# Performance work log

Measured on AMD Instinct MI355X. Metric: run time of the kernel, lower is better.

Reference implementation:

```python
import jax, jax.numpy as jnp
import numpy as np

HIDDEN = 512
HEADS = 8
HEAD_DIM = HIDDEN // HEADS


def setup_inputs() -> dict:
    key = jax.random.key(0)
    ks = jax.random.split(key, 12)
    B, N, C = 4, 2048, HIDDEN
    s = 1.0 / np.sqrt(C)
    inp = {
        "query_content": jax.random.normal(ks[0], (B, N, C), dtype=jnp.float32),
        "query_pos": jax.random.uniform(ks[1], (B, N, 4), dtype=jnp.float32),
        "Wq": jax.random.uniform(ks[2], (C, C), jnp.float32, -s, s),
        "bq": jax.random.uniform(ks[3], (C,), jnp.float32, -s, s),
        "Wk": jax.random.uniform(ks[4], (C, C), jnp.float32, -s, s),
        "bk": jax.random.uniform(ks[5], (C,), jnp.float32, -s, s),
        "Wv": jax.random.uniform(ks[6], (C, C), jnp.float32, -s, s),
        "bv": jax.random.uniform(ks[7], (C,), jnp.float32, -s, s),
        "Wo": jax.random.uniform(ks[8], (C, C), jnp.float32, -s, s),
        "bo": jax.random.uniform(ks[9], (C,), jnp.float32, -s, s),
        "gamma": jnp.ones((C,), jnp.float32),
        "beta": jnp.zeros((C,), jnp.float32),
    }
    return inp


def _iof_bias(query_pos):
    # query_pos: [B, N, 4] -> bias [B, N, N] = -0.1 * sqrt(dx^2 + dy^2 + eps)
    x = query_pos[..., 0]
    y = query_pos[..., 1]
    dx = jnp.abs(x[:, :, None] - x[:, None, :])
    dy = jnp.abs(y[:, :, None] - y[:, None, :])
    dist = jnp.sqrt(dx * dx + dy * dy + 1e-8)
    return -0.1 * dist


def reference(query_content, query_pos, Wq, bq, Wk, bk, Wv, bv, Wo, bo, gamma, beta):
    B, N, C = query_content.shape
    H, D = HEADS, HEAD_DIM
    # torch Linear: x @ W.T + b
    Q = (query_content @ Wq.T + bq).reshape(B, N, H, D).transpose(0, 2, 1, 3)
    K = (query_content @ Wk.T + bk).reshape(B, N, H, D).transpose(0, 2, 1, 3)
    V = (query_content @ Wv.T + bv).reshape(B, N, H, D).transpose(0, 2, 1, 3)
    scores = jnp.einsum("bhnd,bhmd->bhnm", Q, K) / jnp.sqrt(jnp.float32(D))
    scores = scores + _iof_bias(query_pos)[:, None, :, :]
    attn = jax.nn.softmax(scores, axis=-1)
    out = jnp.einsum("bhnm,bhmd->bhnd", attn, V)
    out = out.transpose(0, 2, 1, 3).reshape(B, N, C)
    out = out @ Wo.T + bo
    h = out + query_content
    mu = jnp.mean(h, axis=-1, keepdims=True)
    var = jnp.var(h, axis=-1, keepdims=True)
    return (h - mu) / jnp.sqrt(var + 1e-5) * gamma + beta
```

## Files before the change

### kernel.cpp

```cpp
#include <hip/hip_runtime.h>
#include <hip/hip_bf16.h>

#define C_DIM 512
#define H_NUM 8
#define D_DIM 64
#define B_NUM 4
#define N_SEQ 2048
#define M_TOT (B_NUM*N_SEQ)

typedef unsigned short u16;
typedef unsigned int   u32;
typedef __attribute__((ext_vector_type(8))) short short8;
typedef __attribute__((ext_vector_type(4))) float f32x4;

#define MFMA16 __builtin_amdgcn_mfma_f32_16x16x32_bf16

__device__ __forceinline__ u16 f2b(float f) {
    union { float f; u32 u; } v; v.f = f;
    u32 r = v.u + 0x7FFFu + ((v.u >> 16) & 1u);
    return (u16)(r >> 16);
}
__device__ __forceinline__ float fexp2(float x) {
    float r;
    asm("v_exp_f32 %0, %1" : "=v"(r) : "v"(x));
    return r;
}
__device__ __forceinline__ float b2f_lo(u32 u) {
    union { u32 u; float f; } v; v.u = u << 16; return v.f;
}
__device__ __forceinline__ float b2f_hi(u32 u) {
    union { u32 u; float f; } v; v.u = u & 0xFFFF0000u; return v.f;
}
__device__ __forceinline__ void gload16(const u16* g, u16* l) {
    __builtin_amdgcn_global_load_lds(
        (const __attribute__((address_space(1))) void*)g,
        (__attribute__((address_space(3))) void*)l, 16, 0, 0);
}
__device__ __forceinline__ void cast8(const float* s, u16* d) {
    const float4* p = (const float4*)s;
    float4 a = p[0], b = p[1];
    short8 v;
    v[0] = (short)f2b(a.x); v[1] = (short)f2b(a.y);
    v[2] = (short)f2b(a.z); v[3] = (short)f2b(a.w);
    v[4] = (short)f2b(b.x); v[5] = (short)f2b(b.y);
    v[6] = (short)f2b(b.z); v[7] = (short)f2b(b.w);
    *(short8*)d = v;
}

__global__ __launch_bounds__(256) void k_prep(const float* __restrict__ qc,
                                              const float* __restrict__ Wq,
                                              const float* __restrict__ Wk,
                                              const float* __restrict__ Wv,
                                              const float* __restrict__ Wo,
                                              const float* __restrict__ bq,
                                              const float* __restrict__ bk,
                                              const float* __restrict__ bv,
                                              const float* __restrict__ bo,
                                              const float* __restrict__ qpos,
                                              u16* __restrict__ xb,
                                              u16* __restrict__ wb,
                                              float* __restrict__ bqkv,
                                              u16* __restrict__ bias)
{
    const int bid = blockIdx.x, t = threadIdx.x;
    if (bid < 2048) {
        int i = bid * 256 + t;
        cast8(qc + (size_t)i * 8, xb + (size_t)i * 8);
    } else if (bid < 2560) {
        int r = bid - 2048;
        int y = r >> 7;
        const float* s = (y == 0) ? Wq : (y == 1) ? Wk : (y == 2) ? Wv : Wo;
        int i = (r & 127) * 256 + t;
        cast8(s + (size_t)i * 8, wb + (size_t)y * 262144 + (size_t)i * 8);
    } else if (bid < 2568) {
        int idx = (bid - 2560) * 256 + t;
        float v = idx < 512 ? bq[idx] : idx < 1024 ? bk[idx - 512]
                : idx < 1536 ? bv[idx - 1024] : bo[idx - 1536];
        bqkv[idx] = v;
    } else {
        int r = bid - 2568;
        int i = r & 2047, b = r >> 11;
        const float4 qi = *(const float4*)(qpos + (size_t)(b * 2048 + i) * 4);
        const float4* pj = (const float4*)(qpos + ((size_t)b * 2048 + t * 8) * 4);
        const float NC = -0.1f * 1.4426950408889634f;
        short8 v;
        #pragma unroll
        for (int jj = 0; jj < 8; ++jj) {
            float4 pk = pj[jj];
            float dx = qi.x - pk.x, dy = qi.y - pk.y;
            float d2 = fmaf(dx, dx, fmaf(dy, dy, 1e-8f));
            v[jj] = (short)f2b(sqrtf(d2) * NC);
        }
        *(short8*)(bias + (size_t)(b * 2048 + i) * 2048 + t * 8) = v;
    }
}

__global__ __launch_bounds__(256) void k_gemm(const u16* __restrict__ A,
                                              const u16* __restrict__ Bw,
                                              const float* __restrict__ bias,
                                              u16* __restrict__ oq,
                                              u16* __restrict__ ok,
                                              u16* __restrict__ ov,
                                              float* __restrict__ outf,
                                              int fixed_mode)
{
    __shared__ alignas(16) u16 la[4][128][8];
    __shared__ alignas(16) u16 lb[4][128][8];
    const int t = threadIdx.x;
    const int nwg = gridDim.x * gridDim.y;
    const int wgid = blockIdx.y * gridDim.x + blockIdx.x;
    const int swz = (wgid & 7) * (nwg >> 3) + (wgid >> 3);
    const int ntn = gridDim.y;
    const int m0 = (swz / ntn) * 128, n0 = (swz % ntn) * 128;
    const int w = t >> 6, l = t & 63, lr = l & 15, kg = l >> 4;
    const int wm = w >> 1, wn = w & 1;

    f32x4 acc[4][4] = {};

    const int srow = t & 127;
    const u16* As0 = A + (size_t)(m0 + srow) * C_DIM + (t >> 7) * 8;
    const u16* Bs0 = Bw + (size_t)(n0 + srow) * C_DIM + (t >> 7) * 8;
    u16* ldA = (u16*)la + w * 512;
    u16* ldB = (u16*)lb + w * 512;

    for (int k0 = 0; k0 < C_DIM; k0 += 32) {
        gload16(As0 + k0,      ldA);
        gload16(As0 + k0 + 16, ldA + 2048);
        gload16(Bs0 + k0,      ldB);
        gload16(Bs0 + k0 + 16, ldB + 2048);
        __syncthreads();

        short8 af[4], bf[4];
        #pragma unroll
        for (int fm = 0; fm < 4; ++fm)
            af[fm] = *(const short8*)la[kg][wm * 64 + fm * 16 + lr];
        #pragma unroll
        for (int fn = 0; fn < 4; ++fn)
            bf[fn] = *(const short8*)lb[kg][wn * 64 + fn * 16 + lr];
        #pragma unroll
        for (int fm = 0; fm < 4; ++fm)
        #pragma unroll
        for (int fn = 0; fn < 4; ++fn)
            acc[fm][fn] = MFMA16(af[fm], bf[fn], acc[fm][fn], 0, 0, 0);
        __syncthreads();
    }

    const int mode = (fixed_mode == 3) ? 3 : (n0 >> 9);

    if (mode == 3) {
        #pragma unroll
        for (int fm = 0; fm < 4; ++fm)
        #pragma unroll
        for (int fn = 0; fn < 4; ++fn) {
            int c = n0 + wn * 64 + fn * 16 + lr;
            float bv_ = bias[c];
            #pragma unroll
            for (int i = 0; i < 4; ++i) {
                int m = m0 + wm * 64 + fm * 16 + kg * 4 + i;
                outf[(size_t)m * C_DIM + c] = acc[fm][fn][i] + bv_;
            }
        }
    } else if (mode == 2) {
        #pragma unroll
        for (int fm = 0; fm < 4; ++fm)
        #pragma unroll
        for (int fn = 0; fn < 4; ++fn) {
            int c = n0 + wn * 64 + fn * 16 + lr;
            int cc = c & 511, h = cc >> 6, d = cc & 63;
            float bv_ = bias[c];
            int m = m0 + wm * 64 + fm * 16 + kg * 4;
            int bb = m >> 11, n = m & 2047;
            uint2 pk;
            pk.x = ((u32)f2b(acc[fm][fn][1] + bv_) << 16) | f2b(acc[fm][fn][0] + bv_);
            pk.y = ((u32)f2b(acc[fm][fn][3] + bv_) << 16) | f2b(acc[fm][fn][2] + bv_);
            *(uint2*)(ov + ((size_t)(bb * H_NUM + h) * D_DIM + d) * N_SEQ + n) = pk;
        }
    } else {
        u16* outb = (mode == 0) ? oq : ok;
        #pragma unroll
        for (int fm = 0; fm < 4; ++fm)
        #pragma unroll
        for (int fn = 0; fn < 4; ++fn) {
            int c = n0 + wn * 64 + fn * 16 + lr;
            int cc = c & 511, h = cc >> 6, d = cc & 63;
            float bv_ = bias[c];
            #pragma unroll
            for (int i = 0; i < 4; ++i) {
                int m = m0 + wm * 64 + fm * 16 + kg * 4 + i;
                int bb = m >> 11, n = m & 2047;
                outb[((size_t)(bb * H_NUM + h) * N_SEQ + n) * D_DIM + d] = f2b(bv_ + acc[fm][fn][i]);
            }
        }
    }
}

__global__ __launch_bounds__(512, 4) void k_flash(const u16* __restrict__ Q,
                                                  const u16* __restrict__ K,
                                                  const u16* __restrict__ Vt,
                                                  const u16* __restrict__ bias,
                                                  u16* __restrict__ attn_out)
{
    __shared__ alignas(16) u16 kbuf[3][64][64];
    __shared__ alignas(16) u16 vbuf[3][64][64];
    __shared__ alignas(16) u16 pbuf[8][16][64];

    const int t = threadIdx.x;
    const int w = t >> 6, l = t & 63, lr = l & 15, g = l >> 4;
    const int flat = blockIdx.y * 16 + blockIdx.x;
    const int h = flat >> 6, b = (flat >> 4) & 3, qt = flat & 15;
    const int bh = b * H_NUM + h;
    const int q = qt * 128 + w * 16 + lr;
    const int sx = lr & 7;

    const float SC = 0.125f * 1.4426950408889634f;
    const int NT = N_SEQ / 64;

    const u16* Qb = Q + ((size_t)bh * N_SEQ + q) * D_DIM;
    const u16* Kb = K + (size_t)bh * N_SEQ * D_DIM;
    const u16* Vb = Vt + (size_t)bh * D_DIM * N_SEQ;
    const u16* Bb = bias + ((size_t)b * N_SEQ + q) * N_SEQ;

    short8 aq0 = *(const short8*)(Qb + g * 8);
    short8 aq1 = *(const short8*)(Qb + 32 + g * 8);

    const int sr = t >> 3;
    const int ssl = (t & 7) ^ (sr & 7);
    const u16* gK = Kb + (size_t)sr * D_DIM + ssl * 8;
    const u16* gV = Vb + (size_t)sr * N_SEQ + ssl * 8;

    f32x4 acc[4] = {};
    float lac0 = 0.f, lac1 = 0.f, lac2 = 0.f, lac3 = 0.f;
    uint2 bcur[4], bnxt[4];

    gload16(gK,              (u16*)&kbuf[0][0][0] + w * 512);
    gload16(gV,              (u16*)&vbuf[0][0][0] + w * 512);
    gload16(gK + 64 * D_DIM, (u16*)&kbuf[1][0][0] + w * 512);
    gload16(gV + 64,         (u16*)&vbuf[1][0][0] + w * 512);
    __builtin_amdgcn_sched_barrier(0);
    #pragma unroll
    for (int fn = 0; fn < 4; ++fn)
        bcur[fn] = *(const uint2*)(Bb + fn * 16 + g * 4);
    __builtin_amdgcn_sched_barrier(0);
    asm volatile("s_waitcnt vmcnt(6)" ::: "memory");
    __builtin_amdgcn_s_barrier();

    for (int kt = 0; kt < NT; ++kt) {
        const int bi = kt % 3;
        if (kt + 1 < NT) {
            #pragma unroll
            for (int fn = 0; fn < 4; ++fn)
                bnxt[fn] = *(const uint2*)(Bb + (kt + 1) * 64 + fn * 16 + g * 4);
        }
        __builtin_amdgcn_sched_barrier(0);
        if (kt + 2 < NT) {
            const int bn = (kt + 2) % 3;
            gload16(gK + (size_t)(kt + 2) * 64 * D_DIM, (u16*)&kbuf[bn][0][0] + w * 512);
            gload16(gV + (kt + 2) * 64,                 (u16*)&vbuf[bn][0][0] + w * 512);
        }
        __builtin_amdgcn_sched_barrier(0);

        f32x4 st[4] = {};
        __builtin_amdgcn_s_setprio(1);
        #pragma unroll
        for (int fn = 0; fn < 4; ++fn) {
            short8 ak0 = *(const short8*)&kbuf[bi][fn * 16 + lr][(g ^ sx) * 8];
            short8 ak1 = *(const short8*)&kbuf[bi][fn * 16 + lr][((4 + g) ^ sx) * 8];
            st[fn] = MFMA16(ak0, aq0, st[fn], 0, 0, 0);
            st[fn] = MFMA16(ak1, aq1, st[fn], 0, 0, 0);
        }
        __builtin_amdgcn_s_setprio(0);

        float sv[16];
        #pragma unroll
        for (int fn = 0; fn < 4; ++fn) {
            sv[fn * 4 + 0] = fmaf(st[fn][0], SC, b2f_lo(bcur[fn].x));
            sv[fn * 4 + 1] = fmaf(st[fn][1], SC, b2f_hi(bcur[fn].x));
            sv[fn * 4 + 2] = fmaf(st[fn][2], SC, b2f_lo(bcur[fn].y));
            sv[fn * 4 + 3] = fmaf(st[fn][3], SC, b2f_hi(bcur[fn].y));
        }
        #pragma unroll
        for (int j = 0; j < 4; ++j) { sv[j]      = fexp2(sv[j]);      lac0 += sv[j]; }
        #pragma unroll
        for (int j = 4; j < 8; ++j) { sv[j]      = fexp2(sv[j]);      lac1 += sv[j]; }
        #pragma unroll
        for (int j = 8; j < 12; ++j) { sv[j]     = fexp2(sv[j]);      lac2 += sv[j]; }
        #pragma unroll
        for (int j = 12; j < 16; ++j) { sv[j]    = fexp2(sv[j]);      lac3 += sv[j]; }

        #pragma unroll
        for (int fn = 0; fn < 4; ++fn) {
            union { float f; u32 u; } p0, p1, p2, p3;
            p0.f = sv[fn * 4 + 0]; p1.f = sv[fn * 4 + 1];
            p2.f = sv[fn * 4 + 2]; p3.f = sv[fn * 4 + 3];
            uint2 pk;
            pk.x = (p1.u & 0xFFFF0000u) | (p0.u >> 16);
            pk.y = (p3.u & 0xFFFF0000u) | (p2.u >> 16);
            int slot = fn * 2 + (g >> 1);
            *(uint2*)&pbuf[w][lr][(slot ^ sx) * 8 + (g & 1) * 4] = pk;
        }
        asm volatile("s_waitcnt lgkmcnt(0)" ::: "memory");
        __builtin_amdgcn_sched_barrier(0);

        short8 bp0 = *(const short8*)&pbuf[w][lr][(g ^ sx) * 8];
        short8 bp1 = *(const short8*)&pbuf[w][lr][((4 + g) ^ sx) * 8];

        __builtin_amdgcn_s_setprio(1);
        #pragma unroll
        for (int df = 0; df < 4; ++df) {
            short8 av0 = *(const short8*)&vbuf[bi][df * 16 + lr][(g ^ sx) * 8];
            short8 av1 = *(const short8*)&vbuf[bi][df * 16 + lr][((4 + g) ^ sx) * 8];
            acc[df] = MFMA16(av0, bp0, acc[df], 0, 0, 0);
            acc[df] = MFMA16(av1, bp1, acc[df], 0, 0, 0);
        }
        __builtin_amdgcn_s_setprio(0);

        #pragma unroll
        for (int fn = 0; fn < 4; ++fn) bcur[fn] = bnxt[fn];

        if (kt + 1 < NT) {
            if (kt + 2 < NT) asm volatile("s_waitcnt vmcnt(6)" ::: "memory");
            else             asm volatile("s_waitcnt vmcnt(4)" ::: "memory");
            __builtin_amdgcn_s_barrier();
        }
    }

    float l_run = (lac0 + lac1) + (lac2 + lac3);
    l_run += __shfl_xor(l_run, 16);
    l_run += __shfl_xor(l_run, 32);
    float rl;
    asm("v_rcp_f32 %0, %1" : "=v"(rl) : "v"(l_run));
    rl = rl * (2.f - l_run * rl);
    u16* ob = attn_out + ((size_t)(b * N_SEQ + q)) * C_DIM + h * D_DIM + g * 4;
    #pragma unroll
    for (int df = 0; df < 4; ++df) {
        u32 w0 = ((u32)f2b(acc[df][1] * rl) << 16) | f2b(acc[df][0] * rl);
        u32 w1 = ((u32)f2b(acc[df][3] * rl) << 16) | f2b(acc[df][2] * rl);
        uint2 pk; pk.x = w0; pk.y = w1;
        *(uint2*)(ob + df * 16) = pk;
    }
}

__global__ __launch_bounds__(256) void k_ln(const float* __restrict__ proj,
                                            const float* __restrict__ qc,
                                            const float* __restrict__ gamma,
                                            const float* __restrict__ beta,
                                            float* __restrict__ out)
{
    const int r = blockIdx.x;
    const int t = threadIdx.x;
    const size_t base = (size_t)r * C_DIM;
    float h0 = proj[base + t] + qc[base + t];
    float h1 = proj[base + 256 + t] + qc[base + 256 + t];
    float s = h0 + h1, sq = h0 * h0 + h1 * h1;
    #pragma unroll
    for (int m = 1; m < 64; m <<= 1) {
        s += __shfl_xor(s, m);
        sq += __shfl_xor(sq, m);
    }
    __shared__ float ss[4], ssq[4];
    int w = t >> 6;
    if ((t & 63) == 0) { ss[w] = s; ssq[w] = sq; }
    __syncthreads();
    s = ss[0] + ss[1] + ss[2] + ss[3];
    sq = ssq[0] + ssq[1] + ssq[2] + ssq[3];
    float mu = s * (1.f / C_DIM);
    float var = sq * (1.f / C_DIM) - mu * mu;
    float inv = rsqrtf(var + 1e-5f);
    out[base + t]       = (h0 - mu) * inv * gamma[t] + beta[t];
    out[base + 256 + t] = (h1 - mu) * inv * gamma[256 + t] + beta[256 + t];
}

extern "C" void kernel_launch(void* const* d_in, const int* in_sizes, int n_in,
                              void* d_out, int out_size, void* d_ws, size_t ws_size,
                              hipStream_t stream)
{
    const float* qc    = (const float*)d_in[0];
    const float* qpos  = (const float*)d_in[1];
    const float* Wq    = (const float*)d_in[2];
    const float* bq    = (const float*)d_in[3];
    const float* Wk    = (const float*)d_in[4];
    const float* bk    = (const float*)d_in[5];
    const float* Wv    = (const float*)d_in[6];
    const float* bv    = (const float*)d_in[7];
    const float* Wo    = (const float*)d_in[8];
    const float* bo    = (const float*)d_in[9];
    const float* gamma = (const float*)d_in[10];
    const float* beta  = (const float*)d_in[11];
    float* out = (float*)d_out;

    char* ws = (char*)d_ws;
    const size_t MB = 1024 * 1024;
    u16*   bias_ws = (u16*)(ws);
    u16*   xb_ws   = (u16*)(ws + 32 * MB);
    u16*   wb_ws   = (u16*)(ws + 40 * MB);
    float* bqkv_ws = (float*)(ws + 42 * MB);
    u16*   q_ws    = (u16*)(ws + 43 * MB);
    u16*   k_ws    = (u16*)(ws + 51 * MB);
    u16*   v_ws    = (u16*)(ws + 59 * MB);
    u16*   a_ws    = (u16*)(ws + 75 * MB);
    float* p_ws    = (float*)(ws + 43 * MB);

    k_prep<<<dim3(10760), 256, 0, stream>>>(qc, Wq, Wk, Wv, Wo, bq, bk, bv, bo,
                                            qpos, xb_ws, wb_ws, bqkv_ws, bias_ws);
    k_gemm<<<dim3(M_TOT / 128, 12), 256, 0, stream>>>(xb_ws, wb_ws, bqkv_ws,
                                                      q_ws, k_ws, v_ws, nullptr, -1);
    k_flash<<<dim3(N_SEQ / 128, B_NUM * H_NUM), 512, 0, stream>>>(q_ws, k_ws, v_ws,
                                                                  bias_ws, a_ws);
    k_gemm<<<dim3(M_TOT / 128, 4), 256, 0, stream>>>(a_ws, wb_ws + 1536 * 512,
                                                     bqkv_ws + 1536,
                                                     nullptr, nullptr, nullptr, p_ws, 3);
    k_ln<<<dim3(M_TOT), 256, 0, stream>>>(p_ws, qc, gamma, beta, out);
}
```

Measured before the change: 189.6 us.

## Shrink flash tiles to 64 queries, double-buffer K/V, fuse residual into out-proj

The flash kernel moves from 512-thread blocks over 128 queries to 256-thread blocks over 64 queries. It drops the triple-buffered K/V ring for double buffering with full vmcnt(0) waits, and loads the bias inline instead of prefetching it. The grid is remapped to 8x128 so the batch index follows blockIdx.x. Separately, the residual add of query_content moves into the out-projection GEMM epilogue, so the LayerNorm kernel reads one buffer instead of two. The smaller blocks may raise occupancy and balance, but each K/V tile is now fetched twice as often and the shallower pipeline with full waits exposes more latency.

```diff
diff --git a/kernel.cpp b/kernel.cpp
--- a/kernel.cpp
+++ b/kernel.cpp
@@ -98,6 +98,7 @@
 __global__ __launch_bounds__(256) void k_gemm(const u16* __restrict__ A,
                                               const u16* __restrict__ Bw,
                                               const float* __restrict__ bias,
+                                              const float* __restrict__ qc,
                                               u16* __restrict__ oq,
                                               u16* __restrict__ ok,
                                               u16* __restrict__ ov,
@@ -157,7 +158,7 @@
             #pragma unroll
             for (int i = 0; i < 4; ++i) {
                 int m = m0 + wm * 64 + fm * 16 + kg * 4 + i;
-                outf[(size_t)m * C_DIM + c] = acc[fm][fn][i] + bv_;
+                outf[(size_t)m * C_DIM + c] = acc[fm][fn][i] + bv_ + qc[(size_t)m * C_DIM + c];
             }
         }
     } else if (mode == 2) {
@@ -194,22 +195,24 @@
     }
 }
 
-__global__ __launch_bounds__(512, 4) void k_flash(const u16* __restrict__ Q,
+__global__ __launch_bounds__(256, 4) void k_flash(const u16* __restrict__ Q,
                                                   const u16* __restrict__ K,
                                                   const u16* __restrict__ Vt,
                                                   const u16* __restrict__ bias,
                                                   u16* __restrict__ attn_out)
 {
-    __shared__ alignas(16) u16 kbuf[3][64][64];
-    __shared__ alignas(16) u16 vbuf[3][64][64];
-    __shared__ alignas(16) u16 pbuf[8][16][64];
+    __shared__ alignas(16) u16 kbuf[2][64][64];
+    __shared__ alignas(16) u16 vbuf[2][64][64];
+    __shared__ alignas(16) u16 pbuf[4][16][64];
 
     const int t = threadIdx.x;
     const int w = t >> 6, l = t & 63, lr = l & 15, g = l >> 4;
-    const int flat = blockIdx.y * 16 + blockIdx.x;
-    const int h = flat >> 6, b = (flat >> 4) & 3, qt = flat & 15;
+    const int bx = blockIdx.x, by = blockIdx.y;
+    const int b = bx >> 1;
+    const int i_ = by * 2 + (bx & 1);
+    const int h = i_ >> 5, qt = i_ & 31;
     const int bh = b * H_NUM + h;
-    const int q = qt * 128 + w * 16 + lr;
+    const int q = qt * 64 + w * 16 + lr;
     const int sx = lr & 7;
 
     const float SC = 0.125f * 1.4426950408889634f;
@@ -223,39 +226,40 @@
     short8 aq0 = *(const short8*)(Qb + g * 8);
     short8 aq1 = *(const short8*)(Qb + 32 + g * 8);
 
-    const int sr = t >> 3;
-    const int ssl = (t & 7) ^ (sr & 7);
-    const u16* gK = Kb + (size_t)sr * D_DIM + ssl * 8;
-    const u16* gV = Vb + (size_t)sr * N_SEQ + ssl * 8;
+    const int row0 = t >> 3;
+    const int sl = (t & 7) ^ (row0 & 7);
+    const u16* gK = Kb + (size_t)row0 * D_DIM + sl * 8;
+    const u16* gV = Vb + (size_t)row0 * N_SEQ + sl * 8;
 
     f32x4 acc[4] = {};
     float lac0 = 0.f, lac1 = 0.f, lac2 = 0.f, lac3 = 0.f;
-    uint2 bcur[4], bnxt[4];
-
-    gload16(gK,              (u16*)&kbuf[0][0][0] + w * 512);
-    gload16(gV,              (u16*)&vbuf[0][0][0] + w * 512);
-    gload16(gK + 64 * D_DIM, (u16*)&kbuf[1][0][0] + w * 512);
-    gload16(gV + 64,         (u16*)&vbuf[1][0][0] + w * 512);
-    __builtin_amdgcn_sched_barrier(0);
-    #pragma unroll
-    for (int fn = 0; fn < 4; ++fn)
-        bcur[fn] = *(const uint2*)(Bb + fn * 16 + g * 4);
-    __builtin_amdgcn_sched_barrier(0);
-    asm volatile("s_waitcnt vmcnt(6)" ::: "memory");
+
+    {
+        u16* kd = (u16*)&kbuf[0][0][0] + w * 512;
+        u16* vd = (u16*)&vbuf[0][0][0] + w * 512;
+        gload16(gK, kd);
+        gload16(gK + 32 * D_DIM, kd + 2048);
+        gload16(gV, vd);
+        gload16(gV + (size_t)32 * N_SEQ, vd + 2048);
+    }
+    asm volatile("s_waitcnt vmcnt(0)" ::: "memory");
     __builtin_amdgcn_s_barrier();
 
     for (int kt = 0; kt < NT; ++kt) {
-        const int bi = kt % 3;
+        const int bi = kt & 1;
+        uint2 bld[4];
+        #pragma unroll
+        for (int fn = 0; fn < 4; ++fn)
+            bld[fn] = *(const uint2*)(Bb + kt * 64 + fn * 16 + g * 4);
         if (kt + 1 < NT) {
-            #pragma unroll
-            for (int fn = 0; fn < 4; ++fn)
-                bnxt[fn] = *(const uint2*)(Bb + (kt + 1) * 64 + fn * 16 + g * 4);
-        }
-        __builtin_amdgcn_sched_barrier(0);
-        if (kt + 2 < NT) {
-            const int bn = (kt + 2) % 3;
-            gload16(gK + (size_t)(kt + 2) * 64 * D_DIM, (u16*)&kbuf[bn][0][0] + w * 512);
-            gload16(gV + (kt + 2) * 64,                 (u16*)&vbuf[bn][0][0] + w * 512);
+            u16* kd = (u16*)&kbuf[bi ^ 1][0][0] + w * 512;
+            u16* vd = (u16*)&vbuf[bi ^ 1][0][0] + w * 512;
+            const u16* k1 = gK + (size_t)(kt + 1) * 64 * D_DIM;
+            const u16* v1 = gV + (kt + 1) * 64;
+            gload16(k1, kd);
+            gload16(k1 + 32 * D_DIM, kd + 2048);
+            gload16(v1, vd);
+            gload16(v1 + (size_t)32 * N_SEQ, vd + 2048);
         }
         __builtin_amdgcn_sched_barrier(0);
 
@@ -273,19 +277,19 @@
         float sv[16];
         #pragma unroll
         for (int fn = 0; fn < 4; ++fn) {
-            sv[fn * 4 + 0] = fmaf(st[fn][0], SC, b2f_lo(bcur[fn].x));
-            sv[fn * 4 + 1] = fmaf(st[fn][1], SC, b2f_hi(bcur[fn].x));
-            sv[fn * 4 + 2] = fmaf(st[fn][2], SC, b2f_lo(bcur[fn].y));
-            sv[fn * 4 + 3] = fmaf(st[fn][3], SC, b2f_hi(bcur[fn].y));
-        }
-        #pragma unroll
-        for (int j = 0; j < 4; ++j) { sv[j]      = fexp2(sv[j]);      lac0 += sv[j]; }
-        #pragma unroll
-        for (int j = 4; j < 8; ++j) { sv[j]      = fexp2(sv[j]);      lac1 += sv[j]; }
-        #pragma unroll
-        for (int j = 8; j < 12; ++j) { sv[j]     = fexp2(sv[j]);      lac2 += sv[j]; }
-        #pragma unroll
-        for (int j = 12; j < 16; ++j) { sv[j]    = fexp2(sv[j]);      lac3 += sv[j]; }
+            sv[fn * 4 + 0] = fmaf(st[fn][0], SC, b2f_lo(bld[fn].x));
+            sv[fn * 4 + 1] = fmaf(st[fn][1], SC, b2f_hi(bld[fn].x));
+            sv[fn * 4 + 2] = fmaf(st[fn][2], SC, b2f_lo(bld[fn].y));
+            sv[fn * 4 + 3] = fmaf(st[fn][3], SC, b2f_hi(bld[fn].y));
+        }
+        #pragma unroll
+        for (int j = 0; j < 4; ++j)  { sv[j]  = fexp2(sv[j]);  lac0 += sv[j]; }
+        #pragma unroll
+        for (int j = 4; j < 8; ++j)  { sv[j]  = fexp2(sv[j]);  lac1 += sv[j]; }
+        #pragma unroll
+        for (int j = 8; j < 12; ++j) { sv[j]  = fexp2(sv[j]);  lac2 += sv[j]; }
+        #pragma unroll
+        for (int j = 12; j < 16; ++j){ sv[j]  = fexp2(sv[j]);  lac3 += sv[j]; }
 
         #pragma unroll
         for (int fn = 0; fn < 4; ++fn) {
@@ -314,12 +318,8 @@
         }
         __builtin_amdgcn_s_setprio(0);
 
-        #pragma unroll
-        for (int fn = 0; fn < 4; ++fn) bcur[fn] = bnxt[fn];
-
         if (kt + 1 < NT) {
-            if (kt + 2 < NT) asm volatile("s_waitcnt vmcnt(6)" ::: "memory");
-            else             asm volatile("s_waitcnt vmcnt(4)" ::: "memory");
+            asm volatile("s_waitcnt vmcnt(0)" ::: "memory");
             __builtin_amdgcn_s_barrier();
         }
     }
@@ -340,8 +340,7 @@
     }
 }
 
-__global__ __launch_bounds__(256) void k_ln(const float* __restrict__ proj,
-                                            const float* __restrict__ qc,
+__global__ __launch_bounds__(256) void k_ln(const float* __restrict__ hbuf,
                                             const float* __restrict__ gamma,
                                             const float* __restrict__ beta,
                                             float* __restrict__ out)
@@ -349,8 +348,8 @@
     const int r = blockIdx.x;
     const int t = threadIdx.x;
     const size_t base = (size_t)r * C_DIM;
-    float h0 = proj[base + t] + qc[base + t];
-    float h1 = proj[base + 256 + t] + qc[base + 256 + t];
+    float h0 = hbuf[base + t];
+    float h1 = hbuf[base + 256 + t];
     float s = h0 + h1, sq = h0 * h0 + h1 * h1;
     #pragma unroll
     for (int m = 1; m < 64; m <<= 1) {
@@ -402,12 +401,11 @@
 
     k_prep<<<dim3(10760), 256, 0, stream>>>(qc, Wq, Wk, Wv, Wo, bq, bk, bv, bo,
                                             qpos, xb_ws, wb_ws, bqkv_ws, bias_ws);
-    k_gemm<<<dim3(M_TOT / 128, 12), 256, 0, stream>>>(xb_ws, wb_ws, bqkv_ws,
+    k_gemm<<<dim3(M_TOT / 128, 12), 256, 0, stream>>>(xb_ws, wb_ws, bqkv_ws, nullptr,
                                                       q_ws, k_ws, v_ws, nullptr, -1);
-    k_flash<<<dim3(N_SEQ / 128, B_NUM * H_NUM), 512, 0, stream>>>(q_ws, k_ws, v_ws,
-                                                                  bias_ws, a_ws);
+    k_flash<<<dim3(8, 128), 256, 0, stream>>>(q_ws, k_ws, v_ws, bias_ws, a_ws);
     k_gemm<<<dim3(M_TOT / 128, 4), 256, 0, stream>>>(a_ws, wb_ws + 1536 * 512,
-                                                     bqkv_ws + 1536,
+                                                     bqkv_ws + 1536, qc,
                                                      nullptr, nullptr, nullptr, p_ws, 3);
-    k_ln<<<dim3(M_TOT), 256, 0, stream>>>(p_ws, qc, gamma, beta, out);
-}
+    k_ln<<<dim3(M_TOT), 256, 0, stream>>>(p_ws, gamma, beta, out);
+}
```

Result: slower. 204.7 us (+8.0%).

## Triple-buffer GEMM K-loop and fuse residual add into output projection

Applied to the files above, without the earlier changes.

The GEMM main loop moves from a single shared buffer with two barriers per step to a three-stage ring. Loads run two K-slices ahead, with vmcnt-gated single barriers and raised priority around the MFMA block, so global loads overlap compute. The residual add of query_content moves into the output-projection GEMM epilogue, and the LayerNorm kernel now reads one buffer with float2 vector accesses. The costs are triple the LDS footprint per GEMM workgroup and an extra strided fp32 read in the GEMM epilogue.

```diff
diff --git a/kernel.cpp b/kernel.cpp
--- a/kernel.cpp
+++ b/kernel.cpp
@@ -98,14 +98,15 @@
 __global__ __launch_bounds__(256) void k_gemm(const u16* __restrict__ A,
                                               const u16* __restrict__ Bw,
                                               const float* __restrict__ bias,
+                                              const float* __restrict__ qc,
                                               u16* __restrict__ oq,
                                               u16* __restrict__ ok,
                                               u16* __restrict__ ov,
                                               float* __restrict__ outf,
                                               int fixed_mode)
 {
-    __shared__ alignas(16) u16 la[4][128][8];
-    __shared__ alignas(16) u16 lb[4][128][8];
+    __shared__ alignas(16) u16 la[3][4][128][8];
+    __shared__ alignas(16) u16 lb[3][4][128][8];
     const int t = threadIdx.x;
     const int nwg = gridDim.x * gridDim.y;
     const int wgid = blockIdx.y * gridDim.x + blockIdx.x;
@@ -114,35 +115,59 @@
     const int m0 = (swz / ntn) * 128, n0 = (swz % ntn) * 128;
     const int w = t >> 6, l = t & 63, lr = l & 15, kg = l >> 4;
     const int wm = w >> 1, wn = w & 1;
+    const int NS = C_DIM / 32;
 
     f32x4 acc[4][4] = {};
 
     const int srow = t & 127;
     const u16* As0 = A + (size_t)(m0 + srow) * C_DIM + (t >> 7) * 8;
     const u16* Bs0 = Bw + (size_t)(n0 + srow) * C_DIM + (t >> 7) * 8;
-    u16* ldA = (u16*)la + w * 512;
-    u16* ldB = (u16*)lb + w * 512;
-
-    for (int k0 = 0; k0 < C_DIM; k0 += 32) {
-        gload16(As0 + k0,      ldA);
-        gload16(As0 + k0 + 16, ldA + 2048);
-        gload16(Bs0 + k0,      ldB);
-        gload16(Bs0 + k0 + 16, ldB + 2048);
-        __syncthreads();
+
+    #pragma unroll
+    for (int s = 0; s < 2; ++s) {
+        u16* ldA = (u16*)la[s] + w * 512;
+        u16* ldB = (u16*)lb[s] + w * 512;
+        gload16(As0 + s * 32,      ldA);
+        gload16(As0 + s * 32 + 16, ldA + 2048);
+        gload16(Bs0 + s * 32,      ldB);
+        gload16(Bs0 + s * 32 + 16, ldB + 2048);
+    }
+    asm volatile("s_waitcnt vmcnt(4)" ::: "memory");
+    __builtin_amdgcn_s_barrier();
+
+    for (int s = 0; s < NS; ++s) {
+        const int bi = s % 3;
+        if (s + 2 < NS) {
+            const int bn = (s + 2) % 3;
+            u16* ldA = (u16*)la[bn] + w * 512;
+            u16* ldB = (u16*)lb[bn] + w * 512;
+            gload16(As0 + (s + 2) * 32,      ldA);
+            gload16(As0 + (s + 2) * 32 + 16, ldA + 2048);
+            gload16(Bs0 + (s + 2) * 32,      ldB);
+            gload16(Bs0 + (s + 2) * 32 + 16, ldB + 2048);
+        }
+        __builtin_amdgcn_sched_barrier(0);
 
         short8 af[4], bf[4];
         #pragma unroll
         for (int fm = 0; fm < 4; ++fm)
-            af[fm] = *(const short8*)la[kg][wm * 64 + fm * 16 + lr];
+            af[fm] = *(const short8*)la[bi][kg][wm * 64 + fm * 16 + lr];
         #pragma unroll
         for (int fn = 0; fn < 4; ++fn)
-            bf[fn] = *(const short8*)lb[kg][wn * 64 + fn * 16 + lr];
+            bf[fn] = *(const short8*)lb[bi][kg][wn * 64 + fn * 16 + lr];
+        __builtin_amdgcn_s_setprio(1);
         #pragma unroll
         for (int fm = 0; fm < 4; ++fm)
         #pragma unroll
         for (int fn = 0; fn < 4; ++fn)
             acc[fm][fn] = MFMA16(af[fm], bf[fn], acc[fm][fn], 0, 0, 0);
-        __syncthreads();
+        __builtin_amdgcn_s_setprio(0);
+
+        if (s + 1 < NS) {
+            if (s + 2 < NS) asm volatile("s_waitcnt vmcnt(4)" ::: "memory");
+            else            asm volatile("s_waitcnt vmcnt(0)" ::: "memory");
+            __builtin_amdgcn_s_barrier();
+        }
     }
 
     const int mode = (fixed_mode == 3) ? 3 : (n0 >> 9);
@@ -157,7 +182,7 @@
             #pragma unroll
             for (int i = 0; i < 4; ++i) {
                 int m = m0 + wm * 64 + fm * 16 + kg * 4 + i;
-                outf[(size_t)m * C_DIM + c] = acc[fm][fn][i] + bv_;
+                outf[(size_t)m * C_DIM + c] = acc[fm][fn][i] + bv_ + qc[(size_t)m * C_DIM + c];
             }
         }
     } else if (mode == 2) {
@@ -279,13 +304,13 @@
             sv[fn * 4 + 3] = fmaf(st[fn][3], SC, b2f_hi(bcur[fn].y));
         }
         #pragma unroll
-        for (int j = 0; j < 4; ++j) { sv[j]      = fexp2(sv[j]);      lac0 += sv[j]; }
-        #pragma unroll
-        for (int j = 4; j < 8; ++j) { sv[j]      = fexp2(sv[j]);      lac1 += sv[j]; }
-        #pragma unroll
-        for (int j = 8; j < 12; ++j) { sv[j]     = fexp2(sv[j]);      lac2 += sv[j]; }
-        #pragma unroll
-        for (int j = 12; j < 16; ++j) { sv[j]    = fexp2(sv[j]);      lac3 += sv[j]; }
+        for (int j = 0; j < 4; ++j)  { sv[j]  = fexp2(sv[j]);  lac0 += sv[j]; }
+        #pragma unroll
+        for (int j = 4; j < 8; ++j)  { sv[j]  = fexp2(sv[j]);  lac1 += sv[j]; }
+        #pragma unroll
+        for (int j = 8; j < 12; ++j) { sv[j]  = fexp2(sv[j]);  lac2 += sv[j]; }
+        #pragma unroll
+        for (int j = 12; j < 16; ++j){ sv[j]  = fexp2(sv[j]);  lac3 += sv[j]; }
 
         #pragma unroll
         for (int fn = 0; fn < 4; ++fn) {
@@ -340,8 +365,7 @@
     }
 }
 
-__global__ __launch_bounds__(256) void k_ln(const float* __restrict__ proj,
-                                            const float* __restrict__ qc,
+__global__ __launch_bounds__(256) void k_ln(const float* __restrict__ hbuf,
                                             const float* __restrict__ gamma,
                                             const float* __restrict__ beta,
                                             float* __restrict__ out)
@@ -349,9 +373,8 @@
     const int r = blockIdx.x;
     const int t = threadIdx.x;
     const size_t base = (size_t)r * C_DIM;
-    float h0 = proj[base + t] + qc[base + t];
-    float h1 = proj[base + 256 + t] + qc[base + 256 + t];
-    float s = h0 + h1, sq = h0 * h0 + h1 * h1;
+    float2 h01 = *(const float2*)(hbuf + base + t * 2);
+    float s = h01.x + h01.y, sq = h01.x * h01.x + h01.y * h01.y;
     #pragma unroll
     for (int m = 1; m < 64; m <<= 1) {
         s += __shfl_xor(s, m);
@@ -366,8 +389,12 @@
     float mu = s * (1.f / C_DIM);
     float var = sq * (1.f / C_DIM) - mu * mu;
     float inv = rsqrtf(var + 1e-5f);
-    out[base + t]       = (h0 - mu) * inv * gamma[t] + beta[t];
-    out[base + 256 + t] = (h1 - mu) * inv * gamma[256 + t] + beta[256 + t];
+    float2 g01 = *(const float2*)(gamma + t * 2);
+    float2 b01 = *(const float2*)(beta + t * 2);
+    float2 o;
+    o.x = (h01.x - mu) * inv * g01.x + b01.x;
+    o.y = (h01.y - mu) * inv * g01.y + b01.y;
+    *(float2*)(out + base + t * 2) = o;
 }
 
 extern "C" void kernel_launch(void* const* d_in, const int* in_sizes, int n_in,
@@ -402,12 +429,11 @@
 
     k_prep<<<dim3(10760), 256, 0, stream>>>(qc, Wq, Wk, Wv, Wo, bq, bk, bv, bo,
                                             qpos, xb_ws, wb_ws, bqkv_ws, bias_ws);
-    k_gemm<<<dim3(M_TOT / 128, 12), 256, 0, stream>>>(xb_ws, wb_ws, bqkv_ws,
+    k_gemm<<<dim3(M_TOT / 128, 12), 256, 0, stream>>>(xb_ws, wb_ws, bqkv_ws, nullptr,
                                                       q_ws, k_ws, v_ws, nullptr, -1);
-    k_flash<<<dim3(N_SEQ / 128, B_NUM * H_NUM), 512, 0, stream>>>(q_ws, k_ws, v_ws,
-                                                                  bias_ws, a_ws);
+    k_flash<<<dim3(16, 32), 512, 0, stream>>>(q_ws, k_ws, v_ws, bias_ws, a_ws);
     k_gemm<<<dim3(M_TOT / 128, 4), 256, 0, stream>>>(a_ws, wb_ws + 1536 * 512,
-                                                     bqkv_ws + 1536,
+                                                     bqkv_ws + 1536, qc,
                                                      nullptr, nullptr, nullptr, p_ws, 3);
-    k_ln<<<dim3(M_TOT), 256, 0, stream>>>(p_ws, qc, gamma, beta, out);
-}
+    k_ln<<<dim3(M_TOT), 256, 0, stream>>>(p_ws, gamma, beta, out);
+}
```

Result: faster. 170.3 us (-10.2%).
